# Performance work log

Measured on AMD Instinct MI355X. Metric: run time of the kernel, lower is better.

## Reference

```python
import jax, jax.numpy as jnp
import numpy as np
from jax import lax

# ---- constants mirroring Prediction.__init__ kwargs ----
INP = 608
NUM_CLASSES = 20
ALPHA, BETA = 1.0, 0.5
OBJ_T, CONF_T, LOC_T = 0.6, 0.05, 0.5
NMS_T, SIZE_T, SIGMA = 0.1, 0.0, 0.5
TOP_K = 8
M_CAND = 256          # fixed-size candidate cap for jit-compatible NMS
NEG = -1e9            # sentinel for masked scores
ANCHORS = [[(116, 90), (156, 198), (373, 326)],
           [(30, 61), (62, 45), (59, 119)],
           [(10, 13), (16, 30), (33, 23)]]


def _decode(pred, anchors):
    """pred: (B, A, G, G, 6+C) raw level output -> decoded flat tensors."""
    B, A, G, _, C = pred.shape
    stride = INP // G
    xy = jax.nn.sigmoid(pred[..., 0:2])
    g = jnp.arange(G, dtype=pred.dtype)
    gx, gy = jnp.meshgrid(g, g)                      # gx[i,j]=j, gy[i,j]=i (np.meshgrid 'xy')
    off = jnp.stack([gx, gy], axis=-1)[None, None]   # (1,1,G,G,2)
    xy = ALPHA * xy - 0.5 * (ALPHA - 1.0) + off
    anc = jnp.asarray(anchors, dtype=pred.dtype) / stride  # (A,2) scaled to grid units
    wh = jnp.exp(pred[..., 2:4]) * anc[None, :, None, None, :]
    box = jnp.concatenate([xy, wh], axis=-1) * stride       # back to pixel units
    obj = jax.nn.sigmoid(pred[..., 4])
    loc = jax.nn.sigmoid(pred[..., 5])
    clsp = jax.nn.softmax(pred[..., 6:], axis=-1)
    N = A * G * G
    return (box.reshape(B, N, 4), obj.reshape(B, N),
            loc.reshape(B, N), clsp.reshape(B, N, NUM_CLASSES))


def _soft_nms(boxes, s0, cls):
    """Per-image Gaussian soft-NMS (class-aware), +1 pixel IoU convention as in bbox_iou.
    boxes: (M,4) xyxy, s0: (M,) scores (NEG for invalid), cls: (M,) int. Returns kept mask."""
    M = s0.shape[0]

    def step(carry, _):
        s, kept = carry
        j = jnp.argmax(s)
        do = s[j] >= NMS_T
        kept = kept | ((jnp.arange(M) == j) & do)
        bj = boxes[j]
        ix1 = jnp.maximum(bj[0], boxes[:, 0]); iy1 = jnp.maximum(bj[1], boxes[:, 1])
        ix2 = jnp.minimum(bj[2], boxes[:, 2]); iy2 = jnp.minimum(bj[3], boxes[:, 3])
        inter = jnp.maximum(ix2 - ix1 + 1.0, 0.0) * jnp.maximum(iy2 - iy1 + 1.0, 0.0)
        a1 = (bj[2] - bj[0] + 1.0) * (bj[3] - bj[1] + 1.0)
        a2 = (boxes[:, 2] - boxes[:, 0] + 1.0) * (boxes[:, 3] - boxes[:, 1] + 1.0)
        iou = inter / (a1 + a2 - inter + 1e-16)
        decay = jnp.exp(-(iou * iou) / SIGMA)
        s_new = jnp.where(cls == cls[j], s * decay, s).at[j].set(NEG)
        s = jnp.where(do, s_new, s)
        return (s, kept), None

    (_, kept), _ = lax.scan(step, (s0, jnp.zeros(M, dtype=bool)), None, length=M)
    return kept


def _forward(pred_l0, pred_l1, pred_l2):
    parts = [_decode(p, a) for p, a in zip([pred_l0, pred_l1, pred_l2], ANCHORS)]
    box = jnp.concatenate([p[0] for p in parts], axis=1)   # (B,N,4) xywh
    obj = jnp.concatenate([p[1] for p in parts], axis=1)
    loc = jnp.concatenate([p[2] for p in parts], axis=1)
    clsp = jnp.concatenate([p[3] for p in parts], axis=1)

    cx, cy, w, h = box[..., 0], box[..., 1], box[..., 2], box[..., 3]
    x1 = jnp.clip(cx - w / 2, 0.0, INP); y1 = jnp.clip(cy - h / 2, 0.0, INP)
    x2 = jnp.clip(cx + w / 2, 0.0, INP); y2 = jnp.clip(cy + h / 2, 0.0, INP)
    boxes = jnp.stack([x1, y1, x2, y2], axis=-1)            # (B,N,4) xyxy, clamped

    cls_conf = jnp.max(clsp, axis=-1)
    cls_id = jnp.argmax(clsp, axis=-1)
    area = (x2 - x1) * (y2 - y1)
    valid = ((obj >= OBJ_T) & (area >= INP * INP * SIZE_T)
             & (obj * cls_conf >= CONF_T) & (loc >= LOC_T))
    score = (obj * cls_conf) ** BETA * loc ** (1.0 - BETA)
    masked = jnp.where(valid, score, NEG)

    # fixed-size candidate set per image (descending-score sort + cap)
    vals, idx = lax.top_k(masked, M_CAND)                   # (B,M)
    cboxes = jnp.take_along_axis(boxes, idx[..., None], axis=1)
    ccls = jnp.take_along_axis(cls_id, idx, axis=1)
    s0 = jnp.where(vals > NEG / 2, vals, NEG)

    kept = jax.vmap(_soft_nms)(cboxes, s0, ccls)            # (B,M) bool

    # keep_top_k: top_k among kept, ranked by ORIGINAL (pre-decay) score
    fscore = jnp.where(kept, vals, NEG)
    fvals, fidx = lax.top_k(fscore, TOP_K)                  # (B,TOP_K)
    fboxes = jnp.take_along_axis(cboxes, fidx[..., None], axis=1)
    fcls = jnp.take_along_axis(ccls, fidx, axis=1)
    row = jnp.concatenate([fboxes, fvals[..., None],
                           fcls[..., None].astype(fboxes.dtype)], axis=-1)  # (B,K,6)
    ok = fvals > NEG / 2
    return jnp.where(ok[..., None], row, 0.0)


def setup_inputs() -> dict:
    key = jax.random.key(0)
    k0, k1, k2 = jax.random.split(key, 3)
    return {
        "pred_l0": jax.random.normal(k0, (64, 3, 19, 19, 26), dtype=jnp.float32),
        "pred_l1": jax.random.normal(k1, (64, 3, 38, 38, 26), dtype=jnp.float32),
        "pred_l2": jax.random.normal(k2, (64, 3, 76, 76, 26), dtype=jnp.float32),
    }


def reference(pred_l0, pred_l1, pred_l2):
    return _forward(pred_l0, pred_l1, pred_l2)
```

## Files before the change

### kernel.cpp

```cpp
#include <hip/hip_runtime.h>
#include <climits>

constexpr int kB  = 64;
constexpr int kG0 = 19, kG1 = 38, kG2 = 76;
constexpr int kN0 = 3 * kG0 * kG0;
constexpr int kN1 = 3 * kG1 * kG1;
constexpr int kN2 = 3 * kG2 * kG2;
constexpr int kN  = kN0 + kN1 + kN2;
constexpr int kM  = 256;
constexpr int kTopK = 8;
constexpr float kNEG = -1e9f;

constexpr int kT0 = 5, kT1 = 17, kT2 = 68;
constexpr int kTilesPerImg = kT0 + kT1 + kT2;

__constant__ float c_anchors[3][3][2] = {
    {{116.f, 90.f}, {156.f, 198.f}, {373.f, 326.f}},
    {{30.f, 61.f},  {62.f, 45.f},   {59.f, 119.f}},
    {{10.f, 13.f},  {16.f, 30.f},   {33.f, 23.f}},
};

__device__ __forceinline__ float fexpf(float x) { return __expf(x); }
__device__ __forceinline__ float frcpf(float x) { return __builtin_amdgcn_rcpf(x); }
__device__ __forceinline__ float fsigm(float x) { return frcpf(1.0f + __expf(-x)); }

__device__ __forceinline__ unsigned score_to_key(float s) {
  unsigned fb = __float_as_uint(s);
  unsigned m = (fb & 0x80000000u) ? 0xFFFFFFFFu : 0x80000000u;
  return fb ^ m;
}
__device__ __forceinline__ float key_to_score(unsigned k) {
  unsigned fb = (k & 0x80000000u) ? (k ^ 0x80000000u) : ~k;
  return __uint_as_float(fb);
}

__device__ __forceinline__ const float* cell_ptr(
    const float* p0, const float* p1, const float* p2, int b, int n,
    int& lvl, int& a, int& gi, int& gj, float& stride) {
  const float* src; int G, m;
  if (n < kN0)            { src = p0; G = kG0; lvl = 0; m = n;             stride = 32.f; }
  else if (n < kN0 + kN1) { src = p1; G = kG1; lvl = 1; m = n - kN0;       stride = 16.f; }
  else                    { src = p2; G = kG2; lvl = 2; m = n - kN0 - kN1; stride = 8.f; }
  int gg = G * G;
  a = m / gg;
  int r = m - a * gg;
  gi = r / G;
  gj = r - gi * G;
  return src + (size_t)((((b * 3 + a) * G + gi) * G + gj)) * 26;
}

__device__ __forceinline__ void waveArgmax(float& v, int& i) {
  #pragma unroll
  for (int off = 1; off < 64; off <<= 1) {
    float ov = __shfl_xor(v, off);
    int oi = __shfl_xor(i, off);
    if (ov > v || (ov == v && oi < i)) { v = ov; i = oi; }
  }
}
__device__ __forceinline__ float waveMax(float v) {
  #pragma unroll
  for (int off = 1; off < 64; off <<= 1) v = fmaxf(v, __shfl_xor(v, off));
  return v;
}
__device__ __forceinline__ float sel4f(const float a[4], int q) {
  float r = a[0];
  r = (q == 1) ? a[1] : r;
  r = (q == 2) ? a[2] : r;
  r = (q == 3) ? a[3] : r;
  return r;
}
__device__ __forceinline__ int sel4i(const int a[4], int q) {
  int r = a[0];
  r = (q == 1) ? a[1] : r;
  r = (q == 2) ? a[2] : r;
  r = (q == 3) ? a[3] : r;
  return r;
}

__global__ void zero_kernel(int* __restrict__ cnt) {
  if ((int)threadIdx.x < kB) cnt[threadIdx.x] = 0;
}

__global__ __launch_bounds__(256) void score_kernel(
    const float* __restrict__ p0, const float* __restrict__ p1, const float* __restrict__ p2,
    unsigned long long* __restrict__ pairs, int* __restrict__ cnt)
{
  __shared__ float2 lds2[256 * 13];
  __shared__ int wTot[4];
  __shared__ int sBase;

  int t = threadIdx.x;
  int blk = blockIdx.x;
  int b = blk / kTilesPerImg;
  int r = blk - b * kTilesPerImg;
  const float* slab; int NL, lvlOff, tile;
  if (r < kT0)             { slab = p0; NL = kN0; lvlOff = 0;          tile = r; }
  else if (r < kT0 + kT1)  { slab = p1; NL = kN1; lvlOff = kN0;        tile = r - kT0; }
  else                     { slab = p2; NL = kN2; lvlOff = kN0 + kN1;  tile = r - kT0 - kT1; }
  int cellBase = tile * 256;
  int nc = min(256, NL - cellBase);

  const float2* g2 = (const float2*)(slab + ((size_t)b * NL + cellBase) * 26);
  int totF2 = nc * 13;
  for (int i = t; i < totF2; i += 256) lds2[i] = g2[i];
  __syncthreads();

  bool valid = false;
  unsigned long long pairVal = 0;
  if (t < nc) {
    const float2* c2 = &lds2[t * 13];
    float2 ol = c2[2];
    float obj = fsigm(ol.x);
    float loc = fsigm(ol.y);
    float tch[20];
    #pragma unroll
    for (int j = 0; j < 10; ++j) { float2 v = c2[3 + j]; tch[2*j] = v.x; tch[2*j+1] = v.y; }
    float lm = tch[0];
    #pragma unroll
    for (int c = 1; c < 20; ++c) lm = fmaxf(lm, tch[c]);
    float se = 0.f;
    #pragma unroll
    for (int c = 0; c < 20; ++c) se += fexpf(tch[c] - lm);
    float cls_conf = frcpf(se);
    float conf = obj * cls_conf;
    if (obj >= 0.6f && loc >= 0.5f && conf >= 0.05f) {
      float score = sqrtf(conf) * sqrtf(loc);
      int n = lvlOff + cellBase + t;
      valid = true;
      pairVal = ((unsigned long long)score_to_key(score) << 32) | (unsigned)n;
    }
  }

  int lane = t & 63, wave = t >> 6;
  unsigned long long mask = __ballot(valid);
  int lanePfx = __popcll(mask & ((1ull << lane) - 1ull));
  if (lane == 0) wTot[wave] = __popcll(mask);
  __syncthreads();
  if (t == 0) {
    int tot = wTot[0] + wTot[1] + wTot[2] + wTot[3];
    sBase = (tot > 0) ? atomicAdd(&cnt[b], tot) : 0;
  }
  __syncthreads();
  if (valid) {
    int waveOff = 0;
    #pragma unroll
    for (int q = 0; q < 4; ++q) if (q < wave) waveOff += wTot[q];
    pairs[(size_t)b * kN + sBase + waveOff + lanePfx] = pairVal;
  }
}

__device__ __forceinline__ void findThresholdBin(
    const int* hist, int NB, int needed,
    int& outB, int& outCumAbove, int& outTotal,
    int* shWave, int* shOut)
{
  int tid = threadIdx.x, lane = tid & 63, w = tid >> 6;
  if (tid == 0) { shOut[0] = -1; shOut[1] = 0; }
  int ipt = (NB + 511) / 512;
  int base = tid * ipt;
  int csum = 0;
  for (int i = 0; i < ipt; ++i) { int bn = base + i; if (bn < NB) csum += hist[bn]; }
  int v = csum;
  #pragma unroll
  for (int off = 1; off < 64; off <<= 1) {
    int tv = __shfl_down(v, off);
    if (lane + off < 64) v += tv;
  }
  if (lane == 0) shWave[w] = v;
  __syncthreads();
  int above = 0, total = 0;
  #pragma unroll
  for (int q = 0; q < 8; ++q) {
    int wt = shWave[q];
    total += wt;
    if (q > w) above += wt;
  }
  int S = v + above;
  if (S >= needed && S - csum < needed) {
    int running = S - csum;
    for (int i = ipt - 1; i >= 0; --i) {
      int bn = base + i; if (bn >= NB) continue;
      int c = hist[bn];
      if (running + c >= needed) { shOut[0] = bn; shOut[1] = running; break; }
      running += c;
    }
  }
  __syncthreads();
  outB = shOut[0]; outCumAbove = shOut[1]; outTotal = total;
  __syncthreads();
}

__global__ __launch_bounds__(512) void select_kernel(
    const unsigned long long* __restrict__ pairs, const int* __restrict__ cnt,
    int* __restrict__ candIdx, unsigned* __restrict__ candKey)
{
  int b = blockIdx.x, tid = threadIdx.x;
  const unsigned long long* kk = pairs + (size_t)b * kN;
  int NC = cnt[b];
  const unsigned keyNEG = score_to_key(kNEG);

  __shared__ int hist[4096];
  __shared__ int eqBuf[1024];
  __shared__ int shWave[8], shOut[2];
  __shared__ unsigned sT;
  __shared__ int sCgt;

  for (int i = tid; i < 4096; i += 512) hist[i] = 0;
  __syncthreads();
  for (int x = tid; x < NC; x += 512)
    atomicAdd(&hist[(unsigned)(kk[x] >> 52)], 1);
  __syncthreads();
  int B, cumAbove1, total1;
  findThresholdBin(hist, 4096, kM, B, cumAbove1, total1, shWave, shOut);

  if (total1 < kM) {
    if (tid == 0) { sT = keyNEG; sCgt = total1; }
    __syncthreads();
  } else {
    int needed2 = kM - cumAbove1;
    for (int i = tid; i < 4096; i += 512) hist[i] = 0;
    __syncthreads();
    for (int x = tid; x < NC; x += 512) {
      unsigned k = (unsigned)(kk[x] >> 32);
      if ((int)(k >> 20) == B) atomicAdd(&hist[(k >> 8) & 0xFFF], 1);
    }
    __syncthreads();
    int B2, cumAbove2, total2;
    findThresholdBin(hist, 4096, needed2, B2, cumAbove2, total2, shWave, shOut);
    int prefix24 = (B << 12) | B2;
    int needed3 = needed2 - cumAbove2;

    for (int i = tid; i < 256; i += 512) hist[i] = 0;
    __syncthreads();
    for (int x = tid; x < NC; x += 512) {
      unsigned k = (unsigned)(kk[x] >> 32);
      if ((int)(k >> 8) == prefix24) atomicAdd(&hist[k & 0xFF], 1);
    }
    __syncthreads();
    int B3, cumAbove3, total3;
    findThresholdBin(hist, 256, needed3, B3, cumAbove3, total3, shWave, shOut);
    if (tid == 0) {
      sT = ((unsigned)prefix24 << 8) | (unsigned)B3;
      sCgt = cumAbove1 + cumAbove2 + cumAbove3;
    }
    __syncthreads();
  }

  unsigned T = sT;
  int cgt = sCgt;

  __shared__ int sCnt, eqCnt;
  if (tid == 0) { sCnt = 0; eqCnt = 0; }
  __syncthreads();
  int* ci = candIdx + (size_t)b * kM;
  unsigned* ck = candKey + (size_t)b * kM;
  for (int x = tid; x < NC; x += 512) {
    unsigned long long v = kk[x];
    unsigned k = (unsigned)(v >> 32);
    if (k > T) {
      int p = atomicAdd(&sCnt, 1);
      ci[p] = (int)(unsigned)v; ck[p] = k;
    } else if (k == T && T != keyNEG) {
      int p = atomicAdd(&eqCnt, 1); if (p < 1024) eqBuf[p] = (int)(unsigned)v;
    }
  }
  __syncthreads();

  int needed = kM - cgt;
  if (T == keyNEG) {
    if (tid >= cgt && tid < kM) { ci[tid] = -1; ck[tid] = keyNEG; }
  } else {
    int ce = min(eqCnt, 1024);
    if (ce == needed) {
      if (tid < needed) { ci[cgt + tid] = eqBuf[tid]; ck[cgt + tid] = T; }
    } else if (tid == 0) {
      for (int q = 0; q < needed; ++q) {
        int mv = INT_MAX, mp = 0;
        for (int x = 0; x < ce; ++x) if (eqBuf[x] < mv) { mv = eqBuf[x]; mp = x; }
        ci[cgt + q] = mv; ck[cgt + q] = T; eqBuf[mp] = INT_MAX;
      }
    }
  }
}

__global__ __launch_bounds__(64) void nms_kernel(
    const float* __restrict__ p0, const float* __restrict__ p1, const float* __restrict__ p2,
    const int* __restrict__ candIdx, const unsigned* __restrict__ candKey,
    float* __restrict__ out)
{
  int b = blockIdx.x, lane = threadIdx.x;

  float x1[4], y1[4], x2[4], y2[4], val[4], s[4];
  int cls[4];
  bool kept[4];

  #pragma unroll
  for (int q = 0; q < 4; ++q) {
    int slot = b * kM + q * 64 + lane;
    int n = candIdx[slot];
    float sc = key_to_score(candKey[slot]);
    kept[q] = false;
    x1[q] = y1[q] = x2[q] = y2[q] = 0.f;
    cls[q] = 0; val[q] = sc; s[q] = sc;
    if (n >= 0) {
      int lvl, a, gi, gj; float stride;
      const float* p = cell_ptr(p0, p1, p2, b, n, lvl, a, gi, gj, stride);
      const float2* r2 = (const float2*)p;
      float2 c01 = r2[0], c23 = r2[1];
      float cx = (fsigm(c01.x) + (float)gj) * stride;
      float cy = (fsigm(c01.y) + (float)gi) * stride;
      float w = fexpf(c23.x) * c_anchors[lvl][a][0];
      float h = fexpf(c23.y) * c_anchors[lvl][a][1];
      x1[q] = fminf(fmaxf(cx - 0.5f * w, 0.f), 608.f);
      y1[q] = fminf(fmaxf(cy - 0.5f * h, 0.f), 608.f);
      x2[q] = fminf(fmaxf(cx + 0.5f * w, 0.f), 608.f);
      y2[q] = fminf(fmaxf(cy + 0.5f * h, 0.f), 608.f);
      float lm = -3.4e38f; int mc = 0;
      #pragma unroll
      for (int j = 3; j < 13; ++j) {
        float2 v = r2[j];
        int c0 = 2 * (j - 3);
        if (v.x > lm) { lm = v.x; mc = c0; }
        if (v.y > lm) { lm = v.y; mc = c0 + 1; }
      }
      cls[q] = mc;
    }
  }

  float top8[8];
  #pragma unroll
  for (int i = 0; i < 8; ++i) top8[i] = kNEG;
  int keptCount = 0;

  for (int it = 0; it < kM; ++it) {
    float bv = s[0]; int bq = 0;
    #pragma unroll
    for (int q = 1; q < 4; ++q) if (s[q] > bv) { bv = s[q]; bq = q; }
    int bi = bq * 64 + lane;
    waveArgmax(bv, bi);
    if (bv < 0.1f) break;

    int wlane = bi & 63, wq = bi >> 6;
    float jx1 = __shfl(sel4f(x1, wq), wlane);
    float jy1 = __shfl(sel4f(y1, wq), wlane);
    float jx2 = __shfl(sel4f(x2, wq), wlane);
    float jy2 = __shfl(sel4f(y2, wq), wlane);
    float jval = __shfl(sel4f(val, wq), wlane);
    int   cj  = __shfl(sel4i(cls, wq), wlane);

    float a1 = (jx2 - jx1 + 1.0f) * (jy2 - jy1 + 1.0f);
    #pragma unroll
    for (int q = 0; q < 4; ++q) {
      if (cls[q] == cj) {
        float ix1 = fmaxf(jx1, x1[q]), iy1 = fmaxf(jy1, y1[q]);
        float ix2 = fminf(jx2, x2[q]), iy2 = fminf(jy2, y2[q]);
        float inter = fmaxf(ix2 - ix1 + 1.0f, 0.0f) * fmaxf(iy2 - iy1 + 1.0f, 0.0f);
        float a2 = (x2[q] - x1[q] + 1.0f) * (y2[q] - y1[q] + 1.0f);
        float iou = inter / (a1 + a2 - inter + 1e-16f);
        s[q] *= fexpf(-(iou * iou) * 2.0f);
      }
      if (bi == q * 64 + lane) { kept[q] = true; s[q] = kNEG; }
    }

    float v = jval;
    #pragma unroll
    for (int i = 0; i < 8; ++i) { float m = fmaxf(top8[i], v); v = fminf(top8[i], v); top8[i] = m; }
    ++keptCount;
    if (keptCount >= kTopK) {
      float am = kNEG;
      #pragma unroll
      for (int q = 0; q < 4; ++q) if (s[q] >= 0.1f) am = fmaxf(am, val[q]);
      am = waveMax(am);
      if (am < top8[7]) break;
    }
  }

  float f[4];
  #pragma unroll
  for (int q = 0; q < 4; ++q) f[q] = kept[q] ? val[q] : kNEG;
  for (int k = 0; k < kTopK; ++k) {
    float bv = f[0]; int bq = 0;
    #pragma unroll
    for (int q = 1; q < 4; ++q) if (f[q] > bv) { bv = f[q]; bq = q; }
    int bi = bq * 64 + lane;
    waveArgmax(bv, bi);
    int wlane = bi & 63, wq = bi >> 6;
    if (lane == wlane) {
      float* o = out + (size_t)(b * kTopK + k) * 6;
      if (bv > kNEG * 0.5f) {
        o[0] = sel4f(x1, wq); o[1] = sel4f(y1, wq);
        o[2] = sel4f(x2, wq); o[3] = sel4f(y2, wq);
        o[4] = sel4f(val, wq); o[5] = (float)sel4i(cls, wq);
      } else {
        o[0] = 0.f; o[1] = 0.f; o[2] = 0.f; o[3] = 0.f; o[4] = 0.f; o[5] = 0.f;
      }
    }
    #pragma unroll
    for (int q = 0; q < 4; ++q) if (bi == q * 64 + lane) f[q] = kNEG;
  }
}

extern "C" void kernel_launch(void* const* d_in, const int* in_sizes, int n_in,
                              void* d_out, int out_size, void* d_ws, size_t ws_size,
                              hipStream_t stream) {
  const float* p0 = (const float*)d_in[0];
  const float* p1 = (const float*)d_in[1];
  const float* p2 = (const float*)d_in[2];
  float* out = (float*)d_out;

  unsigned long long* pairs = (unsigned long long*)d_ws;
  int* candIdx = (int*)(pairs + (size_t)kB * kN);
  unsigned* candKey = (unsigned*)(candIdx + kB * kM);
  int* cnt = (int*)(candKey + kB * kM);

  zero_kernel<<<1, 64, 0, stream>>>(cnt);
  score_kernel<<<kB * kTilesPerImg, 256, 0, stream>>>(p0, p1, p2, pairs, cnt);
  select_kernel<<<kB, 512, 0, stream>>>(pairs, cnt, candIdx, candKey);
  nms_kernel<<<kB, 64, 0, stream>>>(p0, p1, p2, candIdx, candKey, out);
}
```

Baseline: 265.6 us.

## Double-buffer score tiles with async global-to-LDS loads over a persistent grid

The score kernel now launches a fixed grid in which each block handles three tiles in turn. The next tile is staged into a second LDS buffer while the current one is scored. Full-size tiles outside level 0 use gfx950's direct global_load_lds 16-byte copies; the others fall back to ordinary copies. This hides load latency behind compute, at the cost of doubling LDS per block, which may lower occupancy, and of depending on barriers to order the async LDS writes.

After: 243.3 us. -8.4%, faster.

```diff
diff --git a/kernel.cpp b/kernel.cpp
--- a/kernel.cpp
+++ b/kernel.cpp
@@ -13,6 +13,8 @@
 
 constexpr int kT0 = 5, kT1 = 17, kT2 = 68;
 constexpr int kTilesPerImg = kT0 + kT1 + kT2;
+constexpr int kGridScore = 1920;
+constexpr int kTilesPerBlk = 3;
 
 __constant__ float c_anchors[3][3][2] = {
     {{116.f, 90.f}, {156.f, 198.f}, {373.f, 326.f}},
@@ -77,6 +79,12 @@
   return r;
 }
 
+__device__ __forceinline__ void async_copy16(const void* g, void* s) {
+  __builtin_amdgcn_global_load_lds(
+      (__attribute__((address_space(1))) unsigned int*)g,
+      (__attribute__((address_space(3))) unsigned int*)s, 16, 0, 0);
+}
+
 __global__ void zero_kernel(int* __restrict__ cnt) {
   if ((int)threadIdx.x < kB) cnt[threadIdx.x] = 0;
 }
@@ -85,67 +93,95 @@
     const float* __restrict__ p0, const float* __restrict__ p1, const float* __restrict__ p2,
     unsigned long long* __restrict__ pairs, int* __restrict__ cnt)
 {
-  __shared__ float2 lds2[256 * 13];
+  __shared__ float2 lds2[2][256 * 13];
   __shared__ int wTot[4];
   __shared__ int sBase;
 
   int t = threadIdx.x;
-  int blk = blockIdx.x;
-  int b = blk / kTilesPerImg;
-  int r = blk - b * kTilesPerImg;
-  const float* slab; int NL, lvlOff, tile;
-  if (r < kT0)             { slab = p0; NL = kN0; lvlOff = 0;          tile = r; }
-  else if (r < kT0 + kT1)  { slab = p1; NL = kN1; lvlOff = kN0;        tile = r - kT0; }
-  else                     { slab = p2; NL = kN2; lvlOff = kN0 + kN1;  tile = r - kT0 - kT1; }
-  int cellBase = tile * 256;
-  int nc = min(256, NL - cellBase);
-
-  const float2* g2 = (const float2*)(slab + ((size_t)b * NL + cellBase) * 26);
-  int totF2 = nc * 13;
-  for (int i = t; i < totF2; i += 256) lds2[i] = g2[i];
-  __syncthreads();
-
-  bool valid = false;
-  unsigned long long pairVal = 0;
-  if (t < nc) {
-    const float2* c2 = &lds2[t * 13];
-    float2 ol = c2[2];
-    float obj = fsigm(ol.x);
-    float loc = fsigm(ol.y);
-    float tch[20];
-    #pragma unroll
-    for (int j = 0; j < 10; ++j) { float2 v = c2[3 + j]; tch[2*j] = v.x; tch[2*j+1] = v.y; }
-    float lm = tch[0];
-    #pragma unroll
-    for (int c = 1; c < 20; ++c) lm = fmaxf(lm, tch[c]);
-    float se = 0.f;
-    #pragma unroll
-    for (int c = 0; c < 20; ++c) se += fexpf(tch[c] - lm);
-    float cls_conf = frcpf(se);
-    float conf = obj * cls_conf;
-    if (obj >= 0.6f && loc >= 0.5f && conf >= 0.05f) {
-      float score = sqrtf(conf) * sqrtf(loc);
-      int n = lvlOff + cellBase + t;
-      valid = true;
-      pairVal = ((unsigned long long)score_to_key(score) << 32) | (unsigned)n;
-    }
-  }
-
   int lane = t & 63, wave = t >> 6;
-  unsigned long long mask = __ballot(valid);
-  int lanePfx = __popcll(mask & ((1ull << lane) - 1ull));
-  if (lane == 0) wTot[wave] = __popcll(mask);
-  __syncthreads();
-  if (t == 0) {
-    int tot = wTot[0] + wTot[1] + wTot[2] + wTot[3];
-    sBase = (tot > 0) ? atomicAdd(&cnt[b], tot) : 0;
-  }
-  __syncthreads();
-  if (valid) {
-    int waveOff = 0;
-    #pragma unroll
-    for (int q = 0; q < 4; ++q) if (q < wave) waveOff += wTot[q];
-    pairs[(size_t)b * kN + sBase + waveOff + lanePfx] = pairVal;
+
+  const float* gb[kTilesPerBlk]; int nc[kTilesPerBlk], n0[kTilesPerBlk], bb[kTilesPerBlk];
+  bool dmaOk[kTilesPerBlk];
+  #pragma unroll
+  for (int j = 0; j < kTilesPerBlk; ++j) {
+    int tileId = (int)blockIdx.x + j * kGridScore;
+    int b = tileId / kTilesPerImg;
+    int r = tileId - b * kTilesPerImg;
+    const float* slab; int NL, lvlOff, tile; bool lvl0 = false;
+    if (r < kT0)            { slab = p0; NL = kN0; lvlOff = 0;         tile = r;            lvl0 = true; }
+    else if (r < kT0 + kT1) { slab = p1; NL = kN1; lvlOff = kN0;       tile = r - kT0; }
+    else                    { slab = p2; NL = kN2; lvlOff = kN0 + kN1; tile = r - kT0 - kT1; }
+    int cellBase = tile * 256;
+    nc[j] = min(256, NL - cellBase);
+    gb[j] = slab + ((size_t)b * NL + cellBase) * 26;
+    n0[j] = lvlOff + cellBase;
+    bb[j] = b;
+    dmaOk[j] = (!lvl0) && (nc[j] == 256);
+  }
+
+  auto stage = [&](int j, int buf) {
+    if (dmaOk[j]) {
+      const char* g = (const char*)gb[j];
+      char* s = (char*)&lds2[buf][0];
+      for (int c = wave; c < 26; c += 4)
+        async_copy16(g + c * 1024 + lane * 16, s + c * 1024);
+    } else {
+      const float2* g2 = (const float2*)gb[j];
+      float2* s2 = &lds2[buf][0];
+      int tot = nc[j] * 13;
+      for (int i = t; i < tot; i += 256) s2[i] = g2[i];
+    }
+  };
+
+  stage(0, 0);
+  #pragma unroll
+  for (int j = 0; j < kTilesPerBlk; ++j) {
+    __syncthreads();
+    if (j + 1 < kTilesPerBlk) stage(j + 1, (j + 1) & 1);
+
+    int curNc = nc[j], curN0 = n0[j], curB = bb[j];
+    const float2* bufp = &lds2[j & 1][0];
+
+    bool valid = false;
+    unsigned long long pairVal = 0;
+    if (t < curNc) {
+      const float2* c2 = &bufp[t * 13];
+      float2 ol = c2[2];
+      float obj = fsigm(ol.x);
+      float loc = fsigm(ol.y);
+      float tch[20];
+      #pragma unroll
+      for (int q = 0; q < 10; ++q) { float2 v = c2[3 + q]; tch[2*q] = v.x; tch[2*q+1] = v.y; }
+      float lm = tch[0];
+      #pragma unroll
+      for (int c = 1; c < 20; ++c) lm = fmaxf(lm, tch[c]);
+      float se = 0.f;
+      #pragma unroll
+      for (int c = 0; c < 20; ++c) se += fexpf(tch[c] - lm);
+      float cls_conf = frcpf(se);
+      float conf = obj * cls_conf;
+      if (obj >= 0.6f && loc >= 0.5f && conf >= 0.05f) {
+        float score = sqrtf(conf) * sqrtf(loc);
+        valid = true;
+        pairVal = ((unsigned long long)score_to_key(score) << 32) | (unsigned)(curN0 + t);
+      }
+    }
+
+    unsigned long long mask = __ballot(valid);
+    int lanePfx = __popcll(mask & ((1ull << lane) - 1ull));
+    if (lane == 0) wTot[wave] = __popcll(mask);
+    __syncthreads();
+    if (t == 0) {
+      int tot = wTot[0] + wTot[1] + wTot[2] + wTot[3];
+      sBase = (tot > 0) ? atomicAdd(&cnt[curB], tot) : 0;
+    }
+    __syncthreads();
+    if (valid) {
+      int waveOff = 0;
+      #pragma unroll
+      for (int q = 0; q < 4; ++q) if (q < wave) waveOff += wTot[q];
+      pairs[(size_t)curB * kN + sBase + waveOff + lanePfx] = pairVal;
+    }
   }
 }
 
@@ -414,7 +450,7 @@
   int* cnt = (int*)(candKey + kB * kM);
 
   zero_kernel<<<1, 64, 0, stream>>>(cnt);
-  score_kernel<<<kB * kTilesPerImg, 256, 0, stream>>>(p0, p1, p2, pairs, cnt);
+  score_kernel<<<kGridScore, 256, 0, stream>>>(p0, p1, p2, pairs, cnt);
   select_kernel<<<kB, 512, 0, stream>>>(pairs, cnt, candIdx, candKey);
   nms_kernel<<<kB, 64, 0, stream>>>(p0, p1, p2, candIdx, candKey, out);
 }
```
